# Kernel tuning notes

Hardware: AMD Instinct MI355X
Metric: run time of the kernel (lower is better)

Reference implementation:

```python
import jax, jax.numpy as jnp
import numpy as np

N_NODES = 50000
N_EDGES = 800000
IN_DIM = 128
HID = 128
BN_EPS = 1e-5


def setup_inputs() -> dict:
    key = jax.random.key(0)
    ks = jax.random.split(key, 8)
    x = jax.random.normal(ks[0], (N_NODES, IN_DIM), dtype=jnp.float32)
    edge_index = jax.random.randint(ks[1], (2, N_EDGES), 0, N_NODES, dtype=jnp.int64)
    s1 = 1.0 / np.sqrt(IN_DIM)
    s2 = 1.0 / np.sqrt(HID)
    return {
        'x': x,
        'edge_index': edge_index,
        'w1_0': jax.random.normal(ks[2], (IN_DIM, HID), dtype=jnp.float32) * s1,
        'b1_0': jnp.zeros((HID,), dtype=jnp.float32),
        'w2_0': jax.random.normal(ks[3], (HID, HID), dtype=jnp.float32) * s2,
        'b2_0': jnp.zeros((HID,), dtype=jnp.float32),
        'g_0': jnp.ones((HID,), dtype=jnp.float32),
        'be_0': jnp.zeros((HID,), dtype=jnp.float32),
        'w1_1': jax.random.normal(ks[4], (HID, HID), dtype=jnp.float32) * s2,
        'b1_1': jnp.zeros((HID,), dtype=jnp.float32),
        'w2_1': jax.random.normal(ks[5], (HID, HID), dtype=jnp.float32) * s2,
        'b2_1': jnp.zeros((HID,), dtype=jnp.float32),
        'g_1': jnp.ones((HID,), dtype=jnp.float32),
        'be_1': jnp.zeros((HID,), dtype=jnp.float32),
    }


def _gin_layer(h, src, dst, w1, b1, w2, b2, g, be):
    # GINConv with eps=0: MLP(h_i + sum_{j->i} h_j); scatter-add over targets
    agg = jax.ops.segment_sum(h[src], dst, num_segments=N_NODES)
    z = h + agg
    z = jax.nn.relu(z @ w1 + b1) @ w2 + b2
    # BatchNorm1d (training mode: batch stats over nodes, biased variance)
    mu = jnp.mean(z, axis=0)
    var = jnp.mean(jnp.square(z - mu), axis=0)
    z = (z - mu) * jax.lax.rsqrt(var + BN_EPS) * g + be
    return jax.nn.relu(z)


def reference(x, edge_index, w1_0, b1_0, w2_0, b2_0, g_0, be_0,
              w1_1, b1_1, w2_1, b2_1, g_1, be_1):
    src, dst = edge_index[0], edge_index[1]
    h = _gin_layer(x, src, dst, w1_0, b1_0, w2_0, b2_0, g_0, be_0)
    # dropout p=0.0 -> no-op between layers
    h = _gin_layer(h, src, dst, w1_1, b1_1, w2_1, b2_1, g_1, be_1)
    return h
```

## Files before the change

### kernel.cpp

```cpp
#include <hip/hip_runtime.h>
#include <hip/hip_bf16.h>

#define HID 128
#define LDA 136
#define BINSH 4
#define BINSZ 16
#define ECAP 512
#define CAP 64

typedef __attribute__((ext_vector_type(8))) short frag8;
typedef __attribute__((ext_vector_type(4))) float f32x4;

__device__ inline float bf2f(unsigned short u) {
    return __uint_as_float(((unsigned int)u) << 16);
}
__device__ inline unsigned short f2bf(float f) {
    __hip_bfloat16 h = __float2bfloat16(f);
    return __builtin_bit_cast(unsigned short, h);
}
__device__ inline ushort4 f4tou4(float4 f) {
    ushort4 u; u.x = f2bf(f.x); u.y = f2bf(f.y); u.z = f2bf(f.z); u.w = f2bf(f.w);
    return u;
}
__device__ inline float4 u4tof4(ushort4 u) {
    return make_float4(bf2f(u.x), bf2f(u.y), bf2f(u.z), bf2f(u.w));
}
__device__ inline float4 bnrelu4(float4 u, float4 s, float4 b) {
    float4 r;
    r.x = fmaxf(fmaf(u.x, s.x, b.x), 0.0f);
    r.y = fmaxf(fmaf(u.y, s.y, b.y), 0.0f);
    r.z = fmaxf(fmaf(u.z, s.z, b.z), 0.0f);
    r.w = fmaxf(fmaf(u.w, s.w, b.w), 0.0f);
    return r;
}
__device__ inline void acc4(float4& a, float4 u) {
    a.x += u.x; a.y += u.y; a.z += u.z; a.w += u.w;
}

__global__ __launch_bounds__(256) void mega_prep_k(
    const float* __restrict__ x, unsigned short* __restrict__ B0,
    const float* __restrict__ w0, const float* __restrict__ w1,
    const float* __restrict__ w2, const float* __restrict__ w3,
    unsigned short* __restrict__ wt,
    const int* __restrict__ src, const int* __restrict__ dst,
    int* __restrict__ binCursorP, int* __restrict__ binned,
    int n_edges, long total4, int fb, int vb)
{
    const int bid = blockIdx.x;
    const int t = threadIdx.x;
    if (bid < fb) {
        int e = bid * 256 + t;
        if (e < n_edges) {
            int d = dst[e];
            int bin = d >> BINSH;
            int p = atomicAdd(&binCursorP[bin * 16], 1);
            if (p < ECAP)
                binned[(size_t)bin * ECAP + p] = (src[e] << BINSH) | (d & (BINSZ - 1));
        }
    } else if (bid < fb + vb) {
        long i = (long)(bid - fb) * 256 + t;
        if (i < total4)
            ((ushort4*)B0)[i] = f4tou4(((const float4*)x)[i]);
    } else {
        int w_id = bid - fb - vb;
        const float* w = (w_id == 0) ? w0 : (w_id == 1) ? w1 : (w_id == 2) ? w2 : w3;
        unsigned short* o = wt + (size_t)w_id * 128 * 128;
        for (int i = 0; i < 64; i++) {
            int idx = t + i * 256;
            int k = idx >> 7, nn = idx & 127;
            o[nn * 128 + k] = f2bf(w[idx]);
        }
    }
}

template<bool BN>
__global__ __launch_bounds__(512) void gather_bin_k(
    const unsigned short* __restrict__ h, unsigned short* __restrict__ z,
    const int* __restrict__ binCursorP, const int* __restrict__ binned,
    const float* __restrict__ S, const float* __restrict__ g,
    const float* __restrict__ be, float inv_n, int n)
{
    __shared__ int Ls[ECAP];
    __shared__ int cnt16[BINSZ];
    __shared__ int perNode[BINSZ * CAP];
    __shared__ float lsc[BN ? 128 : 1], lsh[BN ? 128 : 1];

    const int t = threadIdx.x;
    const int bin = blockIdx.x;
    const int v0 = bin << BINSH;

    if (t < BINSZ) cnt16[t] = 0;
    if (BN && t < 128) {
        float mu = S[t] * inv_n;
        float var = fmaf(-mu, mu, S[128 + t] * inv_n);
        float s = g[t] * rsqrtf(var + 1e-5f);
        lsc[t] = s;
        lsh[t] = fmaf(-mu, s, be[t]);
    }
    int cnt = min(binCursorP[bin * 16], ECAP);
    for (int j = t; j < cnt; j += 512) Ls[j] = binned[(size_t)bin * ECAP + j];
    __syncthreads();

    for (int j = t; j < cnt; j += 512) {
        int pa = Ls[j];
        int node = pa & (BINSZ - 1);
        int p = atomicAdd(&cnt16[node], 1);
        if (p < CAP) perNode[node * CAP + p] = pa >> BINSH;
    }
    __syncthreads();

    const int vl = t >> 5;
    const int v = v0 + vl;
    if (v >= n) return;
    const int q = (t & 31) << 2;

    float4 scv, shv;
    if (BN) {
        scv = *(const float4*)(lsc + q);
        shv = *(const float4*)(lsh + q);
    }

    float4 a0 = u4tof4(*(const ushort4*)(h + (size_t)v * HID + q));
    if (BN) a0 = bnrelu4(a0, scv, shv);
    float4 a1 = make_float4(0.f, 0.f, 0.f, 0.f);

    const int* bucket = perNode + vl * CAP;
    int deg = min(cnt16[vl], CAP);

    int i = 0;
    for (; i + 8 <= deg; i += 8) {
        int s0 = bucket[i + 0], s1 = bucket[i + 1];
        int s2 = bucket[i + 2], s3 = bucket[i + 3];
        int s4 = bucket[i + 4], s5 = bucket[i + 5];
        int s6 = bucket[i + 6], s7 = bucket[i + 7];
        float4 u0 = u4tof4(*(const ushort4*)(h + (size_t)s0 * HID + q));
        float4 u1 = u4tof4(*(const ushort4*)(h + (size_t)s1 * HID + q));
        float4 u2 = u4tof4(*(const ushort4*)(h + (size_t)s2 * HID + q));
        float4 u3 = u4tof4(*(const ushort4*)(h + (size_t)s3 * HID + q));
        float4 u4 = u4tof4(*(const ushort4*)(h + (size_t)s4 * HID + q));
        float4 u5 = u4tof4(*(const ushort4*)(h + (size_t)s5 * HID + q));
        float4 u6 = u4tof4(*(const ushort4*)(h + (size_t)s6 * HID + q));
        float4 u7 = u4tof4(*(const ushort4*)(h + (size_t)s7 * HID + q));
        if (BN) {
            u0 = bnrelu4(u0, scv, shv); u1 = bnrelu4(u1, scv, shv);
            u2 = bnrelu4(u2, scv, shv); u3 = bnrelu4(u3, scv, shv);
            u4 = bnrelu4(u4, scv, shv); u5 = bnrelu4(u5, scv, shv);
            u6 = bnrelu4(u6, scv, shv); u7 = bnrelu4(u7, scv, shv);
        }
        acc4(a0, u0); acc4(a1, u1); acc4(a0, u2); acc4(a1, u3);
        acc4(a0, u4); acc4(a1, u5); acc4(a0, u6); acc4(a1, u7);
    }
    for (; i + 4 <= deg; i += 4) {
        int s0 = bucket[i + 0], s1 = bucket[i + 1];
        int s2 = bucket[i + 2], s3 = bucket[i + 3];
        float4 u0 = u4tof4(*(const ushort4*)(h + (size_t)s0 * HID + q));
        float4 u1 = u4tof4(*(const ushort4*)(h + (size_t)s1 * HID + q));
        float4 u2 = u4tof4(*(const ushort4*)(h + (size_t)s2 * HID + q));
        float4 u3 = u4tof4(*(const ushort4*)(h + (size_t)s3 * HID + q));
        if (BN) {
            u0 = bnrelu4(u0, scv, shv); u1 = bnrelu4(u1, scv, shv);
            u2 = bnrelu4(u2, scv, shv); u3 = bnrelu4(u3, scv, shv);
        }
        acc4(a0, u0); acc4(a1, u1); acc4(a0, u2); acc4(a1, u3);
    }
    for (; i < deg; i++) {
        float4 u = u4tof4(*(const ushort4*)(h + (size_t)bucket[i] * HID + q));
        if (BN) u = bnrelu4(u, scv, shv);
        acc4(a0, u);
    }
    acc4(a0, a1);
    *(ushort4*)(z + (size_t)v * HID + q) = f4tou4(a0);
}

__global__ __launch_bounds__(256) void mlp_k(
    unsigned short* __restrict__ Z,
    const unsigned short* __restrict__ W1t, const float* __restrict__ b1,
    const unsigned short* __restrict__ W2t, const float* __restrict__ b2,
    float* __restrict__ S, int n_rows)
{
    __shared__ unsigned short Hs[128 * LDA];
    __shared__ float red[1024];

    const int t = threadIdx.x;
    const int row0 = blockIdx.x * 128;
    const int wave = t >> 6;
    const int lane = t & 63;
    const int l15  = lane & 15;
    const int quad = lane >> 4;

    const int r0 = row0 + wave * 32 + l15;
    const int r1 = r0 + 16;
    const int rs0 = (r0 < n_rows) ? r0 : 0;
    const int rs1 = (r1 < n_rows) ? r1 : 0;
    frag8 a0[4], a1[4];
    #pragma unroll
    for (int kk = 0; kk < 4; kk++) {
        a0[kk] = *(const frag8*)(Z + (size_t)rs0 * HID + kk * 32 + quad * 8);
        a1[kk] = *(const frag8*)(Z + (size_t)rs1 * HID + kk * 32 + quad * 8);
    }

    f32x4 acc[2][8];
    #pragma unroll
    for (int tr = 0; tr < 2; tr++)
        #pragma unroll
        for (int tc = 0; tc < 8; tc++)
            acc[tr][tc] = (f32x4){0.f, 0.f, 0.f, 0.f};

    #pragma unroll
    for (int kk = 0; kk < 4; kk++) {
        int ko = kk * 32 + quad * 8;
        #pragma unroll
        for (int tc = 0; tc < 8; tc++) {
            frag8 b = *(const frag8*)(W1t + (size_t)(tc * 16 + l15) * HID + ko);
            acc[0][tc] = __builtin_amdgcn_mfma_f32_16x16x32_bf16(a0[kk], b, acc[0][tc], 0, 0, 0);
            acc[1][tc] = __builtin_amdgcn_mfma_f32_16x16x32_bf16(a1[kk], b, acc[1][tc], 0, 0, 0);
        }
    }

    const int wrow = wave * 32;
    #pragma unroll
    for (int tc = 0; tc < 8; tc++) {
        const int col = tc * 16 + l15;
        const float bc = b1[col];
        #pragma unroll
        for (int tr = 0; tr < 2; tr++) {
            #pragma unroll
            for (int r = 0; r < 4; r++) {
                int lrow = wrow + tr * 16 + quad * 4 + r;
                Hs[lrow * LDA + col] = f2bf(fmaxf(acc[tr][tc][r] + bc, 0.f));
            }
        }
    }
    __syncthreads();

    #pragma unroll
    for (int kk = 0; kk < 4; kk++) {
        a0[kk] = *(const frag8*)(Hs + (wave * 32 + l15) * LDA + kk * 32 + quad * 8);
        a1[kk] = *(const frag8*)(Hs + (wave * 32 + 16 + l15) * LDA + kk * 32 + quad * 8);
    }
    #pragma unroll
    for (int tr = 0; tr < 2; tr++)
        #pragma unroll
        for (int tc = 0; tc < 8; tc++)
            acc[tr][tc] = (f32x4){0.f, 0.f, 0.f, 0.f};

    #pragma unroll
    for (int kk = 0; kk < 4; kk++) {
        int ko = kk * 32 + quad * 8;
        #pragma unroll
        for (int tc = 0; tc < 8; tc++) {
            frag8 b = *(const frag8*)(W2t + (size_t)(tc * 16 + l15) * HID + ko);
            acc[0][tc] = __builtin_amdgcn_mfma_f32_16x16x32_bf16(a0[kk], b, acc[0][tc], 0, 0, 0);
            acc[1][tc] = __builtin_amdgcn_mfma_f32_16x16x32_bf16(a1[kk], b, acc[1][tc], 0, 0, 0);
        }
    }

    #pragma unroll
    for (int tc = 0; tc < 8; tc++) {
        const int col = tc * 16 + l15;
        const float bc = b2[col];
        float s = 0.f, sq = 0.f;
        #pragma unroll
        for (int tr = 0; tr < 2; tr++) {
            #pragma unroll
            for (int r = 0; r < 4; r++) {
                int grow = row0 + wrow + tr * 16 + quad * 4 + r;
                float o = acc[tr][tc][r] + bc;
                if (grow < n_rows) {
                    s += o; sq = fmaf(o, o, sq);
                    Z[(size_t)grow * HID + col] = f2bf(o);
                }
            }
        }
        s  += __shfl_xor(s, 16);  s  += __shfl_xor(s, 32);
        sq += __shfl_xor(sq, 16); sq += __shfl_xor(sq, 32);
        if (lane < 16) {
            red[wave * 128 + col] = s;
            red[512 + wave * 128 + col] = sq;
        }
    }
    __syncthreads();
    {
        int which = t >> 7, c = t & 127;
        const float* rp = red + which * 512;
        atomicAdd(&S[which * 128 + c],
                  rp[c] + rp[128 + c] + rp[256 + c] + rp[384 + c]);
    }
}

__global__ __launch_bounds__(256) void bn_apply_f32_k(
    const unsigned short* __restrict__ z, const float* __restrict__ S,
    const float* __restrict__ g, const float* __restrict__ be,
    float* __restrict__ out, float inv_n, long total4)
{
    __shared__ float lsc[128], lsh[128];
    int t = threadIdx.x;
    if (t < 128) {
        float mu = S[t] * inv_n;
        float var = fmaf(-mu, mu, S[128 + t] * inv_n);
        float s = g[t] * rsqrtf(var + 1e-5f);
        lsc[t] = s;
        lsh[t] = fmaf(-mu, s, be[t]);
    }
    __syncthreads();

    long i = blockIdx.x * 256L + t;
    if (i >= total4) return;
    float4 v = u4tof4(((const ushort4*)z)[i]);
    int c0 = ((int)(i & 31)) * 4;
    v.x = fmaxf(fmaf(v.x, lsc[c0 + 0], lsh[c0 + 0]), 0.0f);
    v.y = fmaxf(fmaf(v.y, lsc[c0 + 1], lsh[c0 + 1]), 0.0f);
    v.z = fmaxf(fmaf(v.z, lsc[c0 + 2], lsh[c0 + 2]), 0.0f);
    v.w = fmaxf(fmaf(v.w, lsc[c0 + 3], lsh[c0 + 3]), 0.0f);
    ((float4*)out)[i] = v;
}

extern "C" void kernel_launch(void* const* d_in, const int* in_sizes, int n_in,
                              void* d_out, int out_size, void* d_ws, size_t ws_size,
                              hipStream_t stream)
{
    const float* x    = (const float*)d_in[0];
    const int*   ei   = (const int*)d_in[1];
    const float* w1_0 = (const float*)d_in[2];
    const float* b1_0 = (const float*)d_in[3];
    const float* w2_0 = (const float*)d_in[4];
    const float* b2_0 = (const float*)d_in[5];
    const float* g_0  = (const float*)d_in[6];
    const float* be_0 = (const float*)d_in[7];
    const float* w1_1 = (const float*)d_in[8];
    const float* b1_1 = (const float*)d_in[9];
    const float* w2_1 = (const float*)d_in[10];
    const float* b2_1 = (const float*)d_in[11];
    const float* g_1  = (const float*)d_in[12];
    const float* be_1 = (const float*)d_in[13];
    float* OUT = (float*)d_out;

    const int n       = in_sizes[0] / HID;
    const int n_edges = in_sizes[1] / 2;
    const int* src = ei;
    const int* dst = ei + n_edges;
    const float inv_n = 1.0f / (float)n;
    const int n_bins = (n + BINSZ - 1) / BINSZ;

    char* p = (char*)d_ws;
    unsigned short* B0 = (unsigned short*)p;  p += (size_t)n * HID * sizeof(short);
    unsigned short* B1 = (unsigned short*)p;  p += (size_t)n * HID * sizeof(short);
    unsigned short* Wt = (unsigned short*)p;  p += (size_t)4 * 128 * 128 * sizeof(short);
    int*   binCursorP = (int*)p;  p += (size_t)n_bins * 16 * sizeof(int);
    float* S0         = (float*)p;  p += 256 * sizeof(float);
    float* S1         = (float*)p;  p += 256 * sizeof(float);
    int*   binned     = (int*)p;    p += (size_t)n_bins * ECAP * sizeof(int);

    dim3 blk(256);
    const long total4 = (long)n * (HID / 4);
    const int vb = (int)((total4 + 255) / 256);
    const int fb = (n_edges + 255) / 256;
    const int mlp_blocks = (n + 127) / 128;

    hipMemsetAsync(binCursorP, 0,
                   (size_t)n_bins * 16 * sizeof(int) + 512 * sizeof(float), stream);
    mega_prep_k<<<fb + vb + 4, blk, 0, stream>>>(
        x, B0, w1_0, w2_0, w1_1, w2_1, Wt, src, dst, binCursorP, binned,
        n_edges, total4, fb, vb);

    gather_bin_k<false><<<n_bins, dim3(512), 0, stream>>>(
        B0, B1, binCursorP, binned, nullptr, nullptr, nullptr, inv_n, n);
    mlp_k<<<mlp_blocks, blk, 0, stream>>>(B1, Wt, b1_0, Wt + 16384, b2_0, S0, n);

    gather_bin_k<true><<<n_bins, dim3(512), 0, stream>>>(
        B1, B0, binCursorP, binned, S0, g_0, be_0, inv_n, n);
    mlp_k<<<mlp_blocks, blk, 0, stream>>>(B0, Wt + 2 * 16384, b1_1,
                                          Wt + 3 * 16384, b2_1, S1, n);
    bn_apply_f32_k<<<vb, blk, 0, stream>>>(B0, S1, g_1, be_1, OUT, inv_n, total4);
}
```

Measured before the change: 283.9 us.

## Apply first linear before aggregation and shard edge binning counters

Uses linearity, (h+A h)W1 = hW1 + A(hW1), so the first matmul now runs before the gather. The gather adds bias and ReLU, and the second matmul plus batch statistics runs in a separate kernel. The BN of the previous layer is folded into the next first-GEMM's operand load, and weights are converted into shared memory per block instead of in a prep pass. Edge binning atomics are spread over 8 shards with per-shard capacity 128, which cuts contention but drops edges if a shard overflows. The change adds one extra kernel launch per layer and re-converts weights in every block.

```diff
diff --git a/kernel.cpp b/kernel.cpp
--- a/kernel.cpp
+++ b/kernel.cpp
@@ -5,6 +5,9 @@
 #define LDA 136
 #define BINSH 4
 #define BINSZ 16
+#define NSHARD 8
+#define SHSTRIDE 4096
+#define SCAP 128
 #define ECAP 512
 #define CAP 64
 
@@ -18,90 +21,140 @@
     __hip_bfloat16 h = __float2bfloat16(f);
     return __builtin_bit_cast(unsigned short, h);
 }
+__device__ inline float4 u4tof4(ushort4 u) {
+    return make_float4(bf2f(u.x), bf2f(u.y), bf2f(u.z), bf2f(u.w));
+}
 __device__ inline ushort4 f4tou4(float4 f) {
     ushort4 u; u.x = f2bf(f.x); u.y = f2bf(f.y); u.z = f2bf(f.z); u.w = f2bf(f.w);
     return u;
 }
-__device__ inline float4 u4tof4(ushort4 u) {
-    return make_float4(bf2f(u.x), bf2f(u.y), bf2f(u.z), bf2f(u.w));
-}
-__device__ inline float4 bnrelu4(float4 u, float4 s, float4 b) {
-    float4 r;
-    r.x = fmaxf(fmaf(u.x, s.x, b.x), 0.0f);
-    r.y = fmaxf(fmaf(u.y, s.y, b.y), 0.0f);
-    r.z = fmaxf(fmaf(u.z, s.z, b.z), 0.0f);
-    r.w = fmaxf(fmaf(u.w, s.w, b.w), 0.0f);
-    return r;
-}
 __device__ inline void acc4(float4& a, float4 u) {
     a.x += u.x; a.y += u.y; a.z += u.z; a.w += u.w;
 }
+__device__ inline frag8 f32_frag(const float* p) {
+    float4 u = *(const float4*)p;
+    float4 v = *(const float4*)(p + 4);
+    frag8 f;
+    f[0] = (short)f2bf(u.x); f[1] = (short)f2bf(u.y);
+    f[2] = (short)f2bf(u.z); f[3] = (short)f2bf(u.w);
+    f[4] = (short)f2bf(v.x); f[5] = (short)f2bf(v.y);
+    f[6] = (short)f2bf(v.z); f[7] = (short)f2bf(v.w);
+    return f;
+}
 
 __global__ __launch_bounds__(256) void mega_prep_k(
-    const float* __restrict__ x, unsigned short* __restrict__ B0,
-    const float* __restrict__ w0, const float* __restrict__ w1,
-    const float* __restrict__ w2, const float* __restrict__ w3,
-    unsigned short* __restrict__ wt,
+    const float* __restrict__ x, const float* __restrict__ w1,
+    unsigned short* __restrict__ Y0,
     const int* __restrict__ src, const int* __restrict__ dst,
-    int* __restrict__ binCursorP, int* __restrict__ binned,
-    int n_edges, long total4, int fb, int vb)
+    int* __restrict__ binCursor, int* __restrict__ binned,
+    int n_edges, int n_rows, int fb)
 {
     const int bid = blockIdx.x;
     const int t = threadIdx.x;
+
     if (bid < fb) {
+        const int shard = bid & (NSHARD - 1);
         int e = bid * 256 + t;
         if (e < n_edges) {
             int d = dst[e];
             int bin = d >> BINSH;
-            int p = atomicAdd(&binCursorP[bin * 16], 1);
-            if (p < ECAP)
-                binned[(size_t)bin * ECAP + p] = (src[e] << BINSH) | (d & (BINSZ - 1));
-        }
-    } else if (bid < fb + vb) {
-        long i = (long)(bid - fb) * 256 + t;
-        if (i < total4)
-            ((ushort4*)B0)[i] = f4tou4(((const float4*)x)[i]);
-    } else {
-        int w_id = bid - fb - vb;
-        const float* w = (w_id == 0) ? w0 : (w_id == 1) ? w1 : (w_id == 2) ? w2 : w3;
-        unsigned short* o = wt + (size_t)w_id * 128 * 128;
-        for (int i = 0; i < 64; i++) {
-            int idx = t + i * 256;
-            int k = idx >> 7, nn = idx & 127;
-            o[nn * 128 + k] = f2bf(w[idx]);
-        }
-    }
-}
-
-template<bool BN>
-__global__ __launch_bounds__(512) void gather_bin_k(
-    const unsigned short* __restrict__ h, unsigned short* __restrict__ z,
-    const int* __restrict__ binCursorP, const int* __restrict__ binned,
-    const float* __restrict__ S, const float* __restrict__ g,
-    const float* __restrict__ be, float inv_n, int n)
+            int p = atomicAdd(&binCursor[shard * SHSTRIDE + bin], 1);
+            if (p < SCAP)
+                binned[((size_t)bin * NSHARD + shard) * SCAP + p] =
+                    (src[e] << BINSH) | (d & (BINSZ - 1));
+        }
+        return;
+    }
+
+    __shared__ unsigned short Ws[128 * LDA];
+    const int row0 = (bid - fb) * 128;
+
+    #pragma unroll
+    for (int i = 0; i < 64; i++) {
+        int idx = t + i * 256;
+        Ws[(idx & 127) * LDA + (idx >> 7)] = f2bf(w1[idx]);
+    }
+    __syncthreads();
+
+    const int wave = t >> 6;
+    const int lane = t & 63;
+    const int l15  = lane & 15;
+    const int quad = lane >> 4;
+
+    const int r0 = row0 + wave * 32 + l15;
+    const int r1 = r0 + 16;
+    const int rs0 = (r0 < n_rows) ? r0 : 0;
+    const int rs1 = (r1 < n_rows) ? r1 : 0;
+    frag8 a0[4], a1[4];
+    #pragma unroll
+    for (int kk = 0; kk < 4; kk++) {
+        a0[kk] = f32_frag(x + (size_t)rs0 * HID + kk * 32 + quad * 8);
+        a1[kk] = f32_frag(x + (size_t)rs1 * HID + kk * 32 + quad * 8);
+    }
+
+    f32x4 acc[2][8];
+    #pragma unroll
+    for (int tr = 0; tr < 2; tr++)
+        #pragma unroll
+        for (int tc = 0; tc < 8; tc++)
+            acc[tr][tc] = (f32x4){0.f, 0.f, 0.f, 0.f};
+
+    #pragma unroll
+    for (int kk = 0; kk < 4; kk++) {
+        int ko = kk * 32 + quad * 8;
+        #pragma unroll
+        for (int tc = 0; tc < 8; tc++) {
+            frag8 b = *(const frag8*)(Ws + (tc * 16 + l15) * LDA + ko);
+            acc[0][tc] = __builtin_amdgcn_mfma_f32_16x16x32_bf16(a0[kk], b, acc[0][tc], 0, 0, 0);
+            acc[1][tc] = __builtin_amdgcn_mfma_f32_16x16x32_bf16(a1[kk], b, acc[1][tc], 0, 0, 0);
+        }
+    }
+
+    const int wrow = row0 + wave * 32;
+    #pragma unroll
+    for (int tc = 0; tc < 8; tc++) {
+        const int col = tc * 16 + l15;
+        #pragma unroll
+        for (int tr = 0; tr < 2; tr++)
+            #pragma unroll
+            for (int r = 0; r < 4; r++) {
+                int grow = wrow + tr * 16 + quad * 4 + r;
+                if (grow < n_rows)
+                    Y0[(size_t)grow * HID + col] = f2bf(acc[tr][tc][r]);
+            }
+    }
+}
+
+__global__ __launch_bounds__(512) void gather_k(
+    const unsigned short* __restrict__ Y, unsigned short* __restrict__ H,
+    const int* __restrict__ binCursor, const int* __restrict__ binned,
+    const float* __restrict__ b1, int n)
 {
     __shared__ int Ls[ECAP];
     __shared__ int cnt16[BINSZ];
     __shared__ int perNode[BINSZ * CAP];
-    __shared__ float lsc[BN ? 128 : 1], lsh[BN ? 128 : 1];
+    __shared__ float bsh[128];
 
     const int t = threadIdx.x;
     const int bin = blockIdx.x;
     const int v0 = bin << BINSH;
 
     if (t < BINSZ) cnt16[t] = 0;
-    if (BN && t < 128) {
-        float mu = S[t] * inv_n;
-        float var = fmaf(-mu, mu, S[128 + t] * inv_n);
-        float s = g[t] * rsqrtf(var + 1e-5f);
-        lsc[t] = s;
-        lsh[t] = fmaf(-mu, s, be[t]);
-    }
-    int cnt = min(binCursorP[bin * 16], ECAP);
-    for (int j = t; j < cnt; j += 512) Ls[j] = binned[(size_t)bin * ECAP + j];
-    __syncthreads();
-
-    for (int j = t; j < cnt; j += 512) {
+    if (t < 128) bsh[t] = b1[t];
+
+    int total = 0;
+    #pragma unroll
+    for (int s = 0; s < NSHARD; s++) {
+        int c = min(binCursor[s * SHSTRIDE + bin], SCAP);
+        int avail = ECAP - total;
+        int take = min(c, avail);
+        const int* seg = binned + ((size_t)bin * NSHARD + s) * SCAP;
+        for (int j = t; j < take; j += 512) Ls[total + j] = seg[j];
+        total += take;
+    }
+    __syncthreads();
+
+    for (int j = t; j < total; j += 512) {
         int pa = Ls[j];
         int node = pa & (BINSZ - 1);
         int p = atomicAdd(&cnt16[node], 1);
@@ -114,14 +167,7 @@
     if (v >= n) return;
     const int q = (t & 31) << 2;
 
-    float4 scv, shv;
-    if (BN) {
-        scv = *(const float4*)(lsc + q);
-        shv = *(const float4*)(lsh + q);
-    }
-
-    float4 a0 = u4tof4(*(const ushort4*)(h + (size_t)v * HID + q));
-    if (BN) a0 = bnrelu4(a0, scv, shv);
+    float4 a0 = u4tof4(*(const ushort4*)(Y + (size_t)v * HID + q));
     float4 a1 = make_float4(0.f, 0.f, 0.f, 0.f);
 
     const int* bucket = perNode + vl * CAP;
@@ -133,56 +179,53 @@
         int s2 = bucket[i + 2], s3 = bucket[i + 3];
         int s4 = bucket[i + 4], s5 = bucket[i + 5];
         int s6 = bucket[i + 6], s7 = bucket[i + 7];
-        float4 u0 = u4tof4(*(const ushort4*)(h + (size_t)s0 * HID + q));
-        float4 u1 = u4tof4(*(const ushort4*)(h + (size_t)s1 * HID + q));
-        float4 u2 = u4tof4(*(const ushort4*)(h + (size_t)s2 * HID + q));
-        float4 u3 = u4tof4(*(const ushort4*)(h + (size_t)s3 * HID + q));
-        float4 u4 = u4tof4(*(const ushort4*)(h + (size_t)s4 * HID + q));
-        float4 u5 = u4tof4(*(const ushort4*)(h + (size_t)s5 * HID + q));
-        float4 u6 = u4tof4(*(const ushort4*)(h + (size_t)s6 * HID + q));
-        float4 u7 = u4tof4(*(const ushort4*)(h + (size_t)s7 * HID + q));
-        if (BN) {
-            u0 = bnrelu4(u0, scv, shv); u1 = bnrelu4(u1, scv, shv);
-            u2 = bnrelu4(u2, scv, shv); u3 = bnrelu4(u3, scv, shv);
-            u4 = bnrelu4(u4, scv, shv); u5 = bnrelu4(u5, scv, shv);
-            u6 = bnrelu4(u6, scv, shv); u7 = bnrelu4(u7, scv, shv);
-        }
-        acc4(a0, u0); acc4(a1, u1); acc4(a0, u2); acc4(a1, u3);
-        acc4(a0, u4); acc4(a1, u5); acc4(a0, u6); acc4(a1, u7);
+        acc4(a0, u4tof4(*(const ushort4*)(Y + (size_t)s0 * HID + q)));
+        acc4(a1, u4tof4(*(const ushort4*)(Y + (size_t)s1 * HID + q)));
+        acc4(a0, u4tof4(*(const ushort4*)(Y + (size_t)s2 * HID + q)));
+        acc4(a1, u4tof4(*(const ushort4*)(Y + (size_t)s3 * HID + q)));
+        acc4(a0, u4tof4(*(const ushort4*)(Y + (size_t)s4 * HID + q)));
+        acc4(a1, u4tof4(*(const ushort4*)(Y + (size_t)s5 * HID + q)));
+        acc4(a0, u4tof4(*(const ushort4*)(Y + (size_t)s6 * HID + q)));
+        acc4(a1, u4tof4(*(const ushort4*)(Y + (size_t)s7 * HID + q)));
     }
     for (; i + 4 <= deg; i += 4) {
         int s0 = bucket[i + 0], s1 = bucket[i + 1];
         int s2 = bucket[i + 2], s3 = bucket[i + 3];
-        float4 u0 = u4tof4(*(const ushort4*)(h + (size_t)s0 * HID + q));
-        float4 u1 = u4tof4(*(const ushort4*)(h + (size_t)s1 * HID + q));
-        float4 u2 = u4tof4(*(const ushort4*)(h + (size_t)s2 * HID + q));
-        float4 u3 = u4tof4(*(const ushort4*)(h + (size_t)s3 * HID + q));
-        if (BN) {
-            u0 = bnrelu4(u0, scv, shv); u1 = bnrelu4(u1, scv, shv);
-            u2 = bnrelu4(u2, scv, shv); u3 = bnrelu4(u3, scv, shv);
-        }
-        acc4(a0, u0); acc4(a1, u1); acc4(a0, u2); acc4(a1, u3);
-    }
-    for (; i < deg; i++) {
-        float4 u = u4tof4(*(const ushort4*)(h + (size_t)bucket[i] * HID + q));
-        if (BN) u = bnrelu4(u, scv, shv);
-        acc4(a0, u);
-    }
+        acc4(a0, u4tof4(*(const ushort4*)(Y + (size_t)s0 * HID + q)));
+        acc4(a1, u4tof4(*(const ushort4*)(Y + (size_t)s1 * HID + q)));
+        acc4(a0, u4tof4(*(const ushort4*)(Y + (size_t)s2 * HID + q)));
+        acc4(a1, u4tof4(*(const ushort4*)(Y + (size_t)s3 * HID + q)));
+    }
+    for (; i < deg; i++)
+        acc4(a0, u4tof4(*(const ushort4*)(Y + (size_t)bucket[i] * HID + q)));
+
     acc4(a0, a1);
-    *(ushort4*)(z + (size_t)v * HID + q) = f4tou4(a0);
-}
-
-__global__ __launch_bounds__(256) void mlp_k(
-    unsigned short* __restrict__ Z,
-    const unsigned short* __restrict__ W1t, const float* __restrict__ b1,
-    const unsigned short* __restrict__ W2t, const float* __restrict__ b2,
-    float* __restrict__ S, int n_rows)
-{
-    __shared__ unsigned short Hs[128 * LDA];
+    float4 bv = *(const float4*)(bsh + q);
+    float4 o;
+    o.x = fmaxf(a0.x + bv.x, 0.f);
+    o.y = fmaxf(a0.y + bv.y, 0.f);
+    o.z = fmaxf(a0.z + bv.z, 0.f);
+    o.w = fmaxf(a0.w + bv.w, 0.f);
+    *(ushort4*)(H + (size_t)v * HID + q) = f4tou4(o);
+}
+
+__global__ __launch_bounds__(256) void gemm2_k(
+    unsigned short* __restrict__ Z, const float* __restrict__ w2,
+    const float* __restrict__ b2, float* __restrict__ S, int n_rows)
+{
+    __shared__ unsigned short Ws[128 * LDA];
     __shared__ float red[1024];
 
     const int t = threadIdx.x;
     const int row0 = blockIdx.x * 128;
+
+    #pragma unroll
+    for (int i = 0; i < 64; i++) {
+        int idx = t + i * 256;
+        Ws[(idx & 127) * LDA + (idx >> 7)] = f2bf(w2[idx]);
+    }
+    __syncthreads();
+
     const int wave = t >> 6;
     const int lane = t & 63;
     const int l15  = lane & 15;
@@ -211,57 +254,20 @@
         int ko = kk * 32 + quad * 8;
         #pragma unroll
         for (int tc = 0; tc < 8; tc++) {
-            frag8 b = *(const frag8*)(W1t + (size_t)(tc * 16 + l15) * HID + ko);
+            frag8 b = *(const frag8*)(Ws + (tc * 16 + l15) * LDA + ko);
             acc[0][tc] = __builtin_amdgcn_mfma_f32_16x16x32_bf16(a0[kk], b, acc[0][tc], 0, 0, 0);
             acc[1][tc] = __builtin_amdgcn_mfma_f32_16x16x32_bf16(a1[kk], b, acc[1][tc], 0, 0, 0);
         }
     }
 
     const int wrow = wave * 32;
-    #pragma unroll
-    for (int tc = 0; tc < 8; tc++) {
-        const int col = tc * 16 + l15;
-        const float bc = b1[col];
-        #pragma unroll
-        for (int tr = 0; tr < 2; tr++) {
-            #pragma unroll
-            for (int r = 0; r < 4; r++) {
-                int lrow = wrow + tr * 16 + quad * 4 + r;
-                Hs[lrow * LDA + col] = f2bf(fmaxf(acc[tr][tc][r] + bc, 0.f));
-            }
-        }
-    }
-    __syncthreads();
-
-    #pragma unroll
-    for (int kk = 0; kk < 4; kk++) {
-        a0[kk] = *(const frag8*)(Hs + (wave * 32 + l15) * LDA + kk * 32 + quad * 8);
-        a1[kk] = *(const frag8*)(Hs + (wave * 32 + 16 + l15) * LDA + kk * 32 + quad * 8);
-    }
-    #pragma unroll
-    for (int tr = 0; tr < 2; tr++)
-        #pragma unroll
-        for (int tc = 0; tc < 8; tc++)
-            acc[tr][tc] = (f32x4){0.f, 0.f, 0.f, 0.f};
-
-    #pragma unroll
-    for (int kk = 0; kk < 4; kk++) {
-        int ko = kk * 32 + quad * 8;
-        #pragma unroll
-        for (int tc = 0; tc < 8; tc++) {
-            frag8 b = *(const frag8*)(W2t + (size_t)(tc * 16 + l15) * HID + ko);
-            acc[0][tc] = __builtin_amdgcn_mfma_f32_16x16x32_bf16(a0[kk], b, acc[0][tc], 0, 0, 0);
-            acc[1][tc] = __builtin_amdgcn_mfma_f32_16x16x32_bf16(a1[kk], b, acc[1][tc], 0, 0, 0);
-        }
-    }
-
     #pragma unroll
     for (int tc = 0; tc < 8; tc++) {
         const int col = tc * 16 + l15;
         const float bc = b2[col];
         float s = 0.f, sq = 0.f;
         #pragma unroll
-        for (int tr = 0; tr < 2; tr++) {
+        for (int tr = 0; tr < 2; tr++)
             #pragma unroll
             for (int r = 0; r < 4; r++) {
                 int grow = row0 + wrow + tr * 16 + quad * 4 + r;
@@ -271,7 +277,6 @@
                     Z[(size_t)grow * HID + col] = f2bf(o);
                 }
             }
-        }
         s  += __shfl_xor(s, 16);  s  += __shfl_xor(s, 32);
         sq += __shfl_xor(sq, 16); sq += __shfl_xor(sq, 32);
         if (lane < 16) {
@@ -285,6 +290,92 @@
         const float* rp = red + which * 512;
         atomicAdd(&S[which * 128 + c],
                   rp[c] + rp[128 + c] + rp[256 + c] + rp[384 + c]);
+    }
+}
+
+__global__ __launch_bounds__(256) void gemm1bn_k(
+    const unsigned short* __restrict__ Z, const float* __restrict__ w1,
+    const float* __restrict__ S, const float* __restrict__ g,
+    const float* __restrict__ be, float inv_n,
+    unsigned short* __restrict__ Y, int n_rows)
+{
+    __shared__ unsigned short Ws[128 * LDA];
+    __shared__ float lsc[128], lsh[128];
+
+    const int t = threadIdx.x;
+    const int row0 = blockIdx.x * 128;
+
+    if (t < 128) {
+        float mu = S[t] * inv_n;
+        float var = fmaf(-mu, mu, S[128 + t] * inv_n);
+        float s = g[t] * rsqrtf(var + 1e-5f);
+        lsc[t] = s;
+        lsh[t] = fmaf(-mu, s, be[t]);
+    }
+    #pragma unroll
+    for (int i = 0; i < 64; i++) {
+        int idx = t + i * 256;
+        Ws[(idx & 127) * LDA + (idx >> 7)] = f2bf(w1[idx]);
+    }
+    __syncthreads();
+
+    const int wave = t >> 6;
+    const int lane = t & 63;
+    const int l15  = lane & 15;
+    const int quad = lane >> 4;
+
+    const int r0 = row0 + wave * 32 + l15;
+    const int r1 = r0 + 16;
+    const int rs0 = (r0 < n_rows) ? r0 : 0;
+    const int rs1 = (r1 < n_rows) ? r1 : 0;
+    frag8 a0[4], a1[4];
+    #pragma unroll
+    for (int kk = 0; kk < 4; kk++) {
+        int ko = kk * 32 + quad * 8;
+        float4 s0 = *(const float4*)(lsc + ko), s1 = *(const float4*)(lsc + ko + 4);
+        float4 h0 = *(const float4*)(lsh + ko), h1 = *(const float4*)(lsh + ko + 4);
+        float sc[8] = {s0.x, s0.y, s0.z, s0.w, s1.x, s1.y, s1.z, s1.w};
+        float sh[8] = {h0.x, h0.y, h0.z, h0.w, h1.x, h1.y, h1.z, h1.w};
+        frag8 ra = *(const frag8*)(Z + (size_t)rs0 * HID + ko);
+        frag8 rb = *(const frag8*)(Z + (size_t)rs1 * HID + ko);
+        #pragma unroll
+        for (int j = 0; j < 8; j++) {
+            ra[j] = (short)f2bf(fmaxf(fmaf(bf2f((unsigned short)ra[j]), sc[j], sh[j]), 0.f));
+            rb[j] = (short)f2bf(fmaxf(fmaf(bf2f((unsigned short)rb[j]), sc[j], sh[j]), 0.f));
+        }
+        a0[kk] = ra; a1[kk] = rb;
+    }
+
+    f32x4 acc[2][8];
+    #pragma unroll
+    for (int tr = 0; tr < 2; tr++)
+        #pragma unroll
+        for (int tc = 0; tc < 8; tc++)
+            acc[tr][tc] = (f32x4){0.f, 0.f, 0.f, 0.f};
+
+    #pragma unroll
+    for (int kk = 0; kk < 4; kk++) {
+        int ko = kk * 32 + quad * 8;
+        #pragma unroll
+        for (int tc = 0; tc < 8; tc++) {
+            frag8 b = *(const frag8*)(Ws + (tc * 16 + l15) * LDA + ko);
+            acc[0][tc] = __builtin_amdgcn_mfma_f32_16x16x32_bf16(a0[kk], b, acc[0][tc], 0, 0, 0);
+            acc[1][tc] = __builtin_amdgcn_mfma_f32_16x16x32_bf16(a1[kk], b, acc[1][tc], 0, 0, 0);
+        }
+    }
+
+    const int wrow = row0 + wave * 32;
+    #pragma unroll
+    for (int tc = 0; tc < 8; tc++) {
+        const int col = tc * 16 + l15;
+        #pragma unroll
+        for (int tr = 0; tr < 2; tr++)
+            #pragma unroll
+            for (int r = 0; r < 4; r++) {
+                int grow = wrow + tr * 16 + quad * 4 + r;
+                if (grow < n_rows)
+                    Y[(size_t)grow * HID + col] = f2bf(acc[tr][tc][r]);
+            }
     }
 }
 
@@ -345,31 +436,28 @@
     char* p = (char*)d_ws;
     unsigned short* B0 = (unsigned short*)p;  p += (size_t)n * HID * sizeof(short);
     unsigned short* B1 = (unsigned short*)p;  p += (size_t)n * HID * sizeof(short);
-    unsigned short* Wt = (unsigned short*)p;  p += (size_t)4 * 128 * 128 * sizeof(short);
-    int*   binCursorP = (int*)p;  p += (size_t)n_bins * 16 * sizeof(int);
-    float* S0         = (float*)p;  p += 256 * sizeof(float);
-    float* S1         = (float*)p;  p += 256 * sizeof(float);
-    int*   binned     = (int*)p;    p += (size_t)n_bins * ECAP * sizeof(int);
+    int*   binCursor = (int*)p;  p += (size_t)NSHARD * SHSTRIDE * sizeof(int);
+    float* S0        = (float*)p;  p += 256 * sizeof(float);
+    float* S1        = (float*)p;  p += 256 * sizeof(float);
+    int*   binned    = (int*)p;    p += (size_t)n_bins * NSHARD * SCAP * sizeof(int);
 
     dim3 blk(256);
     const long total4 = (long)n * (HID / 4);
     const int vb = (int)((total4 + 255) / 256);
     const int fb = (n_edges + 255) / 256;
-    const int mlp_blocks = (n + 127) / 128;
-
-    hipMemsetAsync(binCursorP, 0,
-                   (size_t)n_bins * 16 * sizeof(int) + 512 * sizeof(float), stream);
-    mega_prep_k<<<fb + vb + 4, blk, 0, stream>>>(
-        x, B0, w1_0, w2_0, w1_1, w2_1, Wt, src, dst, binCursorP, binned,
-        n_edges, total4, fb, vb);
-
-    gather_bin_k<false><<<n_bins, dim3(512), 0, stream>>>(
-        B0, B1, binCursorP, binned, nullptr, nullptr, nullptr, inv_n, n);
-    mlp_k<<<mlp_blocks, blk, 0, stream>>>(B1, Wt, b1_0, Wt + 16384, b2_0, S0, n);
-
-    gather_bin_k<true><<<n_bins, dim3(512), 0, stream>>>(
-        B1, B0, binCursorP, binned, S0, g_0, be_0, inv_n, n);
-    mlp_k<<<mlp_blocks, blk, 0, stream>>>(B0, Wt + 2 * 16384, b1_1,
-                                          Wt + 3 * 16384, b2_1, S1, n);
-    bn_apply_f32_k<<<vb, blk, 0, stream>>>(B0, S1, g_1, be_1, OUT, inv_n, total4);
-}
+    const int gb = (n + 127) / 128;
+
+    hipMemsetAsync(binCursor, 0,
+                   (size_t)NSHARD * SHSTRIDE * sizeof(int) + 512 * sizeof(float), stream);
+
+    mega_prep_k<<<fb + gb, blk, 0, stream>>>(
+        x, w1_0, B0, src, dst, binCursor, binned, n_edges, n, fb);
+
+    gather_k<<<n_bins, dim3(512), 0, stream>>>(B0, B1, binCursor, binned, b1_0, n);
+    gemm2_k<<<gb, blk, 0, stream>>>(B1, w2_0, b2_0, S0, n);
+
+    gemm1bn_k<<<gb, blk, 0, stream>>>(B1, w1_1, S0, g_0, be_0, inv_n, B0, n);
+    gather_k<<<n_bins, dim3(512), 0, stream>>>(B0, B1, binCursor, binned, b1_1, n);
+    gemm2_k<<<gb, blk, 0, stream>>>(B1, w2_1, b2_1, S1, n);
+    bn_apply_f32_k<<<vb, blk, 0, stream>>>(B1, S1, g_1, be_1, OUT, inv_n, total4);
+}
```

After: 324.1 us. +14.2%, slower.

## Replace global-atomic edge binning with histogram, scan and stable placement

Applied to the files above, without the earlier changes.

Edge bucketing by destination bin changes from one global atomicAdd per edge into padded fixed-capacity slots to a three-pass counting sort. Each block builds a shared-memory histogram, then column and global scans give offsets, and a placement pass writes a compact binned array. The aim is to remove contended global atomics and the padded ECAP layout, and to replace the memset. The cost is three extra kernel launches, a serial per-column scan over all edge blocks, and reading dst twice.

```diff
diff --git a/kernel.cpp b/kernel.cpp
--- a/kernel.cpp
+++ b/kernel.cpp
@@ -5,7 +5,9 @@
 #define LDA 136
 #define BINSH 4
 #define BINSZ 16
-#define ECAP 512
+#define NBH 3136
+#define EPB 4096
+#define ECAP 768
 #define CAP 64
 
 typedef __attribute__((ext_vector_type(8))) short frag8;
@@ -18,12 +20,12 @@
     __hip_bfloat16 h = __float2bfloat16(f);
     return __builtin_bit_cast(unsigned short, h);
 }
+__device__ inline float4 u4tof4(ushort4 u) {
+    return make_float4(bf2f(u.x), bf2f(u.y), bf2f(u.z), bf2f(u.w));
+}
 __device__ inline ushort4 f4tou4(float4 f) {
     ushort4 u; u.x = f2bf(f.x); u.y = f2bf(f.y); u.z = f2bf(f.z); u.w = f2bf(f.w);
     return u;
-}
-__device__ inline float4 u4tof4(ushort4 u) {
-    return make_float4(bf2f(u.x), bf2f(u.y), bf2f(u.z), bf2f(u.w));
 }
 __device__ inline float4 bnrelu4(float4 u, float4 s, float4 b) {
     float4 r;
@@ -37,46 +39,133 @@
     a.x += u.x; a.y += u.y; a.z += u.z; a.w += u.w;
 }
 
-__global__ __launch_bounds__(256) void mega_prep_k(
+__global__ __launch_bounds__(256) void hist_k(
+    const int* __restrict__ dst, int* __restrict__ Hst,
     const float* __restrict__ x, unsigned short* __restrict__ B0,
     const float* __restrict__ w0, const float* __restrict__ w1,
     const float* __restrict__ w2, const float* __restrict__ w3,
     unsigned short* __restrict__ wt,
-    const int* __restrict__ src, const int* __restrict__ dst,
-    int* __restrict__ binCursorP, int* __restrict__ binned,
-    int n_edges, long total4, int fb, int vb)
-{
+    int n_edges, long total4, int hb, int vb)
+{
+    __shared__ int hist[NBH];
     const int bid = blockIdx.x;
     const int t = threadIdx.x;
-    if (bid < fb) {
-        int e = bid * 256 + t;
-        if (e < n_edges) {
-            int d = dst[e];
-            int bin = d >> BINSH;
-            int p = atomicAdd(&binCursorP[bin * 16], 1);
-            if (p < ECAP)
-                binned[(size_t)bin * ECAP + p] = (src[e] << BINSH) | (d & (BINSZ - 1));
-        }
-    } else if (bid < fb + vb) {
-        long i = (long)(bid - fb) * 256 + t;
+
+    if (bid < hb) {
+        for (int j = t; j < NBH; j += 256) hist[j] = 0;
+        __syncthreads();
+        const int base = bid * EPB;
+        const int cnt = min(EPB, n_edges - base);
+        for (int i = t; i < cnt; i += 256)
+            atomicAdd(&hist[dst[base + i] >> BINSH], 1);
+        __syncthreads();
+        for (int j = t; j < NBH; j += 256)
+            Hst[(size_t)bid * NBH + j] = hist[j];
+    } else if (bid < hb + vb) {
+        long i = (long)(bid - hb) * 256 + t;
         if (i < total4)
             ((ushort4*)B0)[i] = f4tou4(((const float4*)x)[i]);
     } else {
-        int w_id = bid - fb - vb;
+        int w_id = bid - hb - vb;
         const float* w = (w_id == 0) ? w0 : (w_id == 1) ? w1 : (w_id == 2) ? w2 : w3;
         unsigned short* o = wt + (size_t)w_id * 128 * 128;
         for (int i = 0; i < 64; i++) {
             int idx = t + i * 256;
-            int k = idx >> 7, nn = idx & 127;
-            o[nn * 128 + k] = f2bf(w[idx]);
-        }
+            o[(idx & 127) * 128 + (idx >> 7)] = f2bf(w[idx]);
+        }
+    }
+}
+
+__global__ __launch_bounds__(256) void colscan_k(
+    int* __restrict__ Hst, int* __restrict__ colsum, int nblk)
+{
+    int b = blockIdx.x * 256 + threadIdx.x;
+    if (b >= NBH) return;
+    int run = 0;
+    int i = 0;
+    for (; i + 4 <= nblk; i += 4) {
+        int* p0 = &Hst[(size_t)(i + 0) * NBH + b];
+        int* p1 = &Hst[(size_t)(i + 1) * NBH + b];
+        int* p2 = &Hst[(size_t)(i + 2) * NBH + b];
+        int* p3 = &Hst[(size_t)(i + 3) * NBH + b];
+        int v0 = *p0, v1 = *p1, v2 = *p2, v3 = *p3;
+        *p0 = run; run += v0;
+        *p1 = run; run += v1;
+        *p2 = run; run += v2;
+        *p3 = run; run += v3;
+    }
+    for (; i < nblk; i++) {
+        int v = Hst[(size_t)i * NBH + b];
+        Hst[(size_t)i * NBH + b] = run;
+        run += v;
+    }
+    colsum[b] = run;
+}
+
+__global__ __launch_bounds__(1024) void binscan_k(
+    const int* __restrict__ colsum, int* __restrict__ binStart,
+    float* __restrict__ S0, float* __restrict__ S1)
+{
+    __shared__ int s[NBH];
+    __shared__ int c[1024];
+    const int t = threadIdx.x;
+    if (t < 256) S0[t] = 0.f;
+    else if (t < 512) S1[t - 256] = 0.f;
+    for (int j = t; j < NBH; j += 1024) s[j] = colsum[j];
+    __syncthreads();
+
+    int l0 = 0, l1 = 0, l2 = 0, l3 = 0, sum = 0;
+    if (t < NBH / 4) {
+        int b = t * 4;
+        l0 = s[b]; l1 = s[b + 1]; l2 = s[b + 2]; l3 = s[b + 3];
+        sum = l0 + l1 + l2 + l3;
+    }
+    c[t] = sum;
+    __syncthreads();
+    for (int off = 1; off < 1024; off <<= 1) {
+        int v = (t >= off) ? c[t - off] : 0;
+        __syncthreads();
+        c[t] += v;
+        __syncthreads();
+    }
+    if (t < NBH / 4) {
+        int ex = c[t] - sum;
+        int b = t * 4;
+        binStart[b] = ex;
+        binStart[b + 1] = ex + l0;
+        binStart[b + 2] = ex + l0 + l1;
+        binStart[b + 3] = ex + l0 + l1 + l2;
+    }
+}
+
+__global__ __launch_bounds__(256) void place_k(
+    const int* __restrict__ src, const int* __restrict__ dst,
+    const int* __restrict__ Hst, const int* __restrict__ binStart,
+    int* __restrict__ binned, int n_edges)
+{
+    __shared__ int hist[NBH];
+    const int bid = blockIdx.x;
+    const int t = threadIdx.x;
+    for (int j = t; j < NBH; j += 256) hist[j] = 0;
+    __syncthreads();
+    const int base = bid * EPB;
+    const int cnt = min(EPB, n_edges - base);
+    const int* Hrow = Hst + (size_t)bid * NBH;
+    for (int i = t; i < cnt; i += 256) {
+        int e = base + i;
+        int d = dst[e];
+        int bin = d >> BINSH;
+        int r = atomicAdd(&hist[bin], 1);
+        int pos = binStart[bin] + Hrow[bin] + r;
+        binned[pos] = (src[e] << BINSH) | (d & (BINSZ - 1));
     }
 }
 
 template<bool BN>
-__global__ __launch_bounds__(512) void gather_bin_k(
+__global__ __launch_bounds__(512) void gather_k(
     const unsigned short* __restrict__ h, unsigned short* __restrict__ z,
-    const int* __restrict__ binCursorP, const int* __restrict__ binned,
+    const int* __restrict__ binStart, const int* __restrict__ colsum,
+    const int* __restrict__ binned,
     const float* __restrict__ S, const float* __restrict__ g,
     const float* __restrict__ be, float inv_n, int n)
 {
@@ -97,11 +186,12 @@
         lsc[t] = s;
         lsh[t] = fmaf(-mu, s, be[t]);
     }
-    int cnt = min(binCursorP[bin * 16], ECAP);
-    for (int j = t; j < cnt; j += 512) Ls[j] = binned[(size_t)bin * ECAP + j];
-    __syncthreads();
-
-    for (int j = t; j < cnt; j += 512) {
+    const int base = binStart[bin];
+    const int total = min(colsum[bin], ECAP);
+    for (int j = t; j < total; j += 512) Ls[j] = binned[base + j];
+    __syncthreads();
+
+    for (int j = t; j < total; j += 512) {
         int pa = Ls[j];
         int node = pa & (BINSZ - 1);
         int p = atomicAdd(&cnt16[node], 1);
@@ -223,13 +313,12 @@
         const int col = tc * 16 + l15;
         const float bc = b1[col];
         #pragma unroll
-        for (int tr = 0; tr < 2; tr++) {
+        for (int tr = 0; tr < 2; tr++)
             #pragma unroll
             for (int r = 0; r < 4; r++) {
                 int lrow = wrow + tr * 16 + quad * 4 + r;
                 Hs[lrow * LDA + col] = f2bf(fmaxf(acc[tr][tc][r] + bc, 0.f));
             }
-        }
     }
     __syncthreads();
 
@@ -261,7 +350,7 @@
         const float bc = b2[col];
         float s = 0.f, sq = 0.f;
         #pragma unroll
-        for (int tr = 0; tr < 2; tr++) {
+        for (int tr = 0; tr < 2; tr++)
             #pragma unroll
             for (int r = 0; r < 4; r++) {
                 int grow = row0 + wrow + tr * 16 + quad * 4 + r;
@@ -271,7 +360,6 @@
                     Z[(size_t)grow * HID + col] = f2bf(o);
                 }
             }
-        }
         s  += __shfl_xor(s, 16);  s  += __shfl_xor(s, 32);
         sq += __shfl_xor(sq, 16); sq += __shfl_xor(sq, 32);
         if (lane < 16) {
@@ -346,30 +434,31 @@
     unsigned short* B0 = (unsigned short*)p;  p += (size_t)n * HID * sizeof(short);
     unsigned short* B1 = (unsigned short*)p;  p += (size_t)n * HID * sizeof(short);
     unsigned short* Wt = (unsigned short*)p;  p += (size_t)4 * 128 * 128 * sizeof(short);
-    int*   binCursorP = (int*)p;  p += (size_t)n_bins * 16 * sizeof(int);
-    float* S0         = (float*)p;  p += 256 * sizeof(float);
-    float* S1         = (float*)p;  p += 256 * sizeof(float);
-    int*   binned     = (int*)p;    p += (size_t)n_bins * ECAP * sizeof(int);
+    const int nblk = (n_edges + EPB - 1) / EPB;
+    int*   Hst      = (int*)p;   p += (size_t)nblk * NBH * sizeof(int);
+    int*   colsum   = (int*)p;   p += NBH * sizeof(int);
+    int*   binStart = (int*)p;   p += NBH * sizeof(int);
+    float* S0       = (float*)p; p += 256 * sizeof(float);
+    float* S1       = (float*)p; p += 256 * sizeof(float);
+    int*   binned   = (int*)p;   p += (size_t)n_edges * sizeof(int);
 
     dim3 blk(256);
     const long total4 = (long)n * (HID / 4);
     const int vb = (int)((total4 + 255) / 256);
-    const int fb = (n_edges + 255) / 256;
-    const int mlp_blocks = (n + 127) / 128;
-
-    hipMemsetAsync(binCursorP, 0,
-                   (size_t)n_bins * 16 * sizeof(int) + 512 * sizeof(float), stream);
-    mega_prep_k<<<fb + vb + 4, blk, 0, stream>>>(
-        x, B0, w1_0, w2_0, w1_1, w2_1, Wt, src, dst, binCursorP, binned,
-        n_edges, total4, fb, vb);
-
-    gather_bin_k<false><<<n_bins, dim3(512), 0, stream>>>(
-        B0, B1, binCursorP, binned, nullptr, nullptr, nullptr, inv_n, n);
-    mlp_k<<<mlp_blocks, blk, 0, stream>>>(B1, Wt, b1_0, Wt + 16384, b2_0, S0, n);
-
-    gather_bin_k<true><<<n_bins, dim3(512), 0, stream>>>(
-        B1, B0, binCursorP, binned, S0, g_0, be_0, inv_n, n);
-    mlp_k<<<mlp_blocks, blk, 0, stream>>>(B0, Wt + 2 * 16384, b1_1,
-                                          Wt + 3 * 16384, b2_1, S1, n);
+
+    hist_k<<<nblk + vb + 4, blk, 0, stream>>>(
+        dst, Hst, x, B0, w1_0, w2_0, w1_1, w2_1, Wt, n_edges, total4, nblk, vb);
+    colscan_k<<<(NBH + 255) / 256, blk, 0, stream>>>(Hst, colsum, nblk);
+    binscan_k<<<1, dim3(1024), 0, stream>>>(colsum, binStart, S0, S1);
+    place_k<<<nblk, blk, 0, stream>>>(src, dst, Hst, binStart, binned, n_edges);
+
+    gather_k<false><<<n_bins, dim3(512), 0, stream>>>(
+        B0, B1, binStart, colsum, binned, nullptr, nullptr, nullptr, inv_n, n);
+    mlp_k<<<(n + 127) / 128, blk, 0, stream>>>(B1, Wt, b1_0, Wt + 16384, b2_0, S0, n);
+
+    gather_k<true><<<n_bins, dim3(512), 0, stream>>>(
+        B1, B0, binStart, colsum, binned, S0, g_0, be_0, inv_n, n);
+    mlp_k<<<(n + 127) / 128, blk, 0, stream>>>(B0, Wt + 2 * 16384, b1_1,
+                                               Wt + 3 * 16384, b2_1, S1, n);
     bn_apply_f32_k<<<vb, blk, 0, stream>>>(B0, S1, g_1, be_1, OUT, inv_n, total4);
 }
```

After: 284.1 us. About the same (+0.1%).
